# Optimization experiments

Measured on AMD Instinct MI355X. Metric: run time of the kernel, lower is better.

## Reference

```python
import jax, jax.numpy as jnp
import numpy as np

N = 1 << 20          # number of sample points (rays x samples)
ENC = 32             # hash-grid encoded dim (16 levels x 2 features)
HID = 64
GEO = 15


def setup_inputs() -> dict:
    key = jax.random.key(0)
    ks = jax.random.split(key, 16)
    sc = lambda fan_in: 1.0 / np.sqrt(fan_in)
    return {
        "x": jax.random.normal(ks[0], (N, ENC), jnp.float32),
        "d": jax.random.normal(ks[1], (N, ENC), jnp.float32),
        # sigma net: ENC -> 64 -> 64 -> 1+GEO, bias-free, stored [in, out]
        "Ws0": jax.random.normal(ks[2], (ENC, HID), jnp.float32) * sc(ENC),
        "Ws1": jax.random.normal(ks[3], (HID, HID), jnp.float32) * sc(HID),
        "Ws2": jax.random.normal(ks[4], (HID, 1 + GEO), jnp.float32) * sc(HID),
        # color net: ENC+GEO -> 64 -> 64 -> 64 -> 3, bias-free
        "Wc0": jax.random.normal(ks[5], (ENC + GEO, HID), jnp.float32) * sc(ENC + GEO),
        "Wc1": jax.random.normal(ks[6], (HID, HID), jnp.float32) * sc(HID),
        "Wc2": jax.random.normal(ks[7], (HID, HID), jnp.float32) * sc(HID),
        "Wc3": jax.random.normal(ks[8], (HID, 3), jnp.float32) * sc(HID),
    }


def reference(x, d, Ws0, Ws1, Ws2, Wc0, Wc1, Wc2, Wc3):
    # sigma network: ReLU after EVERY layer (including the last, as in source)
    h = x
    for W in (Ws0, Ws1, Ws2):
        h = jax.nn.relu(h @ W)
    sigma = h[..., 0]            # [N]
    geo_feat = h[..., 1:]        # [N, GEO]

    # color network: ReLU on all but last layer, then sigmoid
    h = jnp.concatenate([d, geo_feat], axis=-1)   # [N, ENC+GEO]
    color_ws = (Wc0, Wc1, Wc2, Wc3)
    for i, W in enumerate(color_ws):
        h = h @ W
        if i != len(color_ws) - 1:
            h = jax.nn.relu(h)
    color = jax.nn.sigmoid(h)    # [N, 3]
    return color, sigma
```

## Files before the change

kernel.cpp:

```cpp
#include <hip/hip_runtime.h>
#include <hip/hip_bf16.h>

typedef short s8v __attribute__((ext_vector_type(8)));
typedef float f4v __attribute__((ext_vector_type(4)));

#define MFMA_BF16 __builtin_amdgcn_mfma_f32_16x16x32_bf16

constexpr int OFF_W0T  = 0;
constexpr int OFF_W1T  = 2560;
constexpr int OFF_W2T  = 7168;
constexpr int OFF_WC0T = 8320;
constexpr int OFF_WC1T = 12928;
constexpr int OFF_WC2T = 17536;
constexpr int OFF_WC3T = 22144;
constexpr int OFF_G    = 23168;
constexpr int SMEM_EL  = OFF_G + 8 * 1024;

static __device__ __forceinline__ short bf2s(__hip_bfloat16 h) {
    union { __hip_bfloat16 b; short s; } u; u.b = h; return u.s;
}

__global__ __launch_bounds__(512, 4)
void rf_fused(const void* __restrict__ xv,
              const void* __restrict__ dv,
              const void* __restrict__ Ws0,
              const void* __restrict__ Ws1,
              const void* __restrict__ Ws2,
              const void* __restrict__ Wc0,
              const void* __restrict__ Wc1,
              const void* __restrict__ Wc2,
              const void* __restrict__ Wc3,
              void* __restrict__ outp,
              int npts)
{
    __shared__ __align__(16) short smem[SMEM_EL];
    __shared__ int cls_cnt;
    const int t = threadIdx.x;

    if (t == 0) cls_cnt = 0;
    __syncthreads();
    {
        unsigned short w = ((const unsigned short*)xv)[2 * t];
        int e = (w >> 7) & 0xFF;
        if (e >= 110 && e <= 140) atomicAdd(&cls_cnt, 1);
    }
    __syncthreads();
    const bool isbf = (cls_cnt >= 256);

    auto ldw = [&](const void* p, int idx) -> short {
        if (isbf) return ((const short*)p)[idx];
        return bf2s(__float2bfloat16(((const float*)p)[idx]));
    };

    for (int i = t; i < 2048; i += 512) { int k = i >> 6, n = i & 63; smem[OFF_W0T  + n*40 + k] = ldw(Ws0, i); }
    for (int i = t; i < 4096; i += 512) { int k = i >> 6, n = i & 63; smem[OFF_W1T  + n*72 + k] = ldw(Ws1, i); }
    for (int i = t; i < 1024; i += 512) { int k = i >> 4, n = i & 15; smem[OFF_W2T  + n*72 + k] = ldw(Ws2, i); }
    for (int i = t; i < 4096; i += 512) { int n = i >> 6, k = i & 63; smem[OFF_WC0T + n*72 + k] = (k < 47) ? ldw(Wc0, k*64 + n) : (short)0; }
    for (int i = t; i < 4096; i += 512) { int k = i >> 6, n = i & 63; smem[OFF_WC1T + n*72 + k] = ldw(Wc1, i); }
    for (int i = t; i < 4096; i += 512) { int k = i >> 6, n = i & 63; smem[OFF_WC2T + n*72 + k] = ldw(Wc2, i); }
    for (int i = t; i < 1024; i += 512) { int n = i >> 6, k = i & 63; smem[OFF_WC3T + n*72 + k] = (n < 3) ? ldw(Wc3, k*3 + n) : (short)0; }
    for (int i = t; i < 8192; i += 512) smem[OFF_G + i] = 0;
    __syncthreads();

    const int lane = t & 63;
    const int wv   = t >> 6;
    const int m16  = lane & 15;
    const int q    = lane >> 4;
    short* sG = smem + OFF_G + wv * 1024;

    const f4v zf = {0.f, 0.f, 0.f, 0.f};

    auto loadRow8f = [&](const void* p, int eoff) -> s8v {
        const float* f = (const float*)p + eoff;
        f4v f0 = *(const f4v*)f;
        f4v f1 = *(const f4v*)(f + 4);
        s8v r;
        #pragma unroll
        for (int j = 0; j < 4; j++) {
            r[j]     = bf2s(__float2bfloat16(f0[j]));
            r[j + 4] = bf2s(__float2bfloat16(f1[j]));
        }
        return r;
    };
    auto putOut = [&](int idx, float v) {
        if (isbf) ((short*)outp)[idx] = bf2s(__float2bfloat16(v));
        else      ((float*)outp)[idx] = v;
    };

    auto redist = [&](const f4v (&a)[4], s8v (&fr)[2]) {
        unsigned int P[4][2];
        #pragma unroll
        for (int kt = 0; kt < 4; kt++)
            #pragma unroll
            for (int rp = 0; rp < 2; rp++) {
                float lo = fmaxf(a[kt][2*rp],     0.f);
                float hi = fmaxf(a[kt][2*rp + 1], 0.f);
                union { __hip_bfloat162 b; unsigned int u; } cu;
                cu.b = __float22bfloat162_rn(float2{lo, hi});
                P[kt][rp] = cu.u;
            }
        #pragma unroll
        for (int a2 = 0; a2 < 2; a2++)
            #pragma unroll
            for (int rp = 0; rp < 2; rp++) {
                asm("v_permlane32_swap_b32 %0, %1" : "+v"(P[2*a2][rp]), "+v"(P[2*a2+1][rp]));
                asm("v_permlane16_swap_b32 %0, %1" : "+v"(P[2*a2][rp]), "+v"(P[2*a2+1][rp]));
            }
        #pragma unroll
        for (int kc = 0; kc < 2; kc++) {
            union { unsigned int u[4]; s8v v; } fu;
            fu.u[0] = P[2*kc][0];     fu.u[1] = P[2*kc][1];
            fu.u[2] = P[2*kc + 1][0]; fu.u[3] = P[2*kc + 1][1];
            fr[kc] = fu.v;
        }
    };

    auto layerT = [&](int woff, const s8v (&bf)[2][2], f4v (&out)[2][4]) {
        #pragma unroll
        for (int kt = 0; kt < 4; kt++) {
            s8v a0 = *(const s8v*)(smem + woff + (kt*16 + m16)*72 + q*8);
            s8v a1 = *(const s8v*)(smem + woff + (kt*16 + m16)*72 + 32 + q*8);
            #pragma unroll
            for (int pt = 0; pt < 2; pt++)
                out[pt][kt] = MFMA_BF16(a1, bf[pt][1], MFMA_BF16(a0, bf[pt][0], zf, 0,0,0), 0,0,0);
        }
    };

    const int ntiles = npts / 32;
    const int tstep  = gridDim.x * 8;
    int tile = blockIdx.x * 8 + wv;

    s8v xr[2], dr[2];
    if (isbf && tile < ntiles) {
        #pragma unroll
        for (int pt = 0; pt < 2; pt++) {
            const int off = (tile*32 + pt*16 + m16)*32 + q*8;
            xr[pt] = *(const s8v*)((const short*)xv + off);
            dr[pt] = *(const s8v*)((const short*)dv + off);
        }
    }

    for (; tile < ntiles; tile += tstep) {
        const int r0  = tile * 32;
        const int nxt = tile + tstep;

        s8v xrn[2], drn[2];
        if (isbf && nxt < ntiles) {
            #pragma unroll
            for (int pt = 0; pt < 2; pt++) {
                const int off = (nxt*32 + pt*16 + m16)*32 + q*8;
                xrn[pt] = *(const s8v*)((const short*)xv + off);
                drn[pt] = *(const s8v*)((const short*)dv + off);
            }
        }

        s8v xb[2], db[2];
        if (isbf) {
            xb[0] = xr[0]; xb[1] = xr[1];
            db[0] = dr[0]; db[1] = dr[1];
        } else {
            #pragma unroll
            for (int pt = 0; pt < 2; pt++) {
                const int off = (r0 + pt*16 + m16)*32 + q*8;
                xb[pt] = loadRow8f(xv, off);
                db[pt] = loadRow8f(dv, off);
            }
        }

        f4v acc[2][4];
        s8v bf[2][2];

        #pragma unroll
        for (int kt = 0; kt < 4; kt++) {
            s8v a0 = *(const s8v*)(smem + OFF_W0T + (kt*16 + m16)*40 + q*8);
            #pragma unroll
            for (int pt = 0; pt < 2; pt++)
                acc[pt][kt] = MFMA_BF16(a0, xb[pt], zf, 0,0,0);
        }
        #pragma unroll
        for (int pt = 0; pt < 2; pt++) redist(acc[pt], bf[pt]);

        layerT(OFF_W1T, bf, acc);
        #pragma unroll
        for (int pt = 0; pt < 2; pt++) redist(acc[pt], bf[pt]);

        f4v s3[2];
        {
            s8v c0 = *(const s8v*)(smem + OFF_W2T + m16*72 + q*8);
            s8v c1 = *(const s8v*)(smem + OFF_W2T + m16*72 + 32 + q*8);
            #pragma unroll
            for (int pt = 0; pt < 2; pt++)
                s3[pt] = MFMA_BF16(c1, bf[pt][1], MFMA_BF16(c0, bf[pt][0], zf, 0,0,0), 0,0,0);
        }

        #pragma unroll
        for (int pt = 0; pt < 2; pt++) {
            const int point = pt*16 + m16;
            #pragma unroll
            for (int r = 0; r < 4; r++) {
                float v = fmaxf(s3[pt][r], 0.f);
                if (q*4 + r == 0) {
                    putOut(3*npts + r0 + point, v);
                    sG[point*32 + 15] = 0;
                } else {
                    sG[point*32 + q*4 + r - 1] = bf2s(__float2bfloat16(v));
                }
            }
        }
        asm volatile("" ::: "memory");

        s8v gb[2];
        #pragma unroll
        for (int pt = 0; pt < 2; pt++)
            gb[pt] = *(const s8v*)(sG + (pt*16 + m16)*32 + q*8);
        asm volatile("" ::: "memory");

        #pragma unroll
        for (int pt = 0; pt < 2; pt++) { bf[pt][0] = db[pt]; bf[pt][1] = gb[pt]; }
        layerT(OFF_WC0T, bf, acc);
        #pragma unroll
        for (int pt = 0; pt < 2; pt++) redist(acc[pt], bf[pt]);

        layerT(OFF_WC1T, bf, acc);
        #pragma unroll
        for (int pt = 0; pt < 2; pt++) redist(acc[pt], bf[pt]);

        layerT(OFF_WC2T, bf, acc);
        #pragma unroll
        for (int pt = 0; pt < 2; pt++) redist(acc[pt], bf[pt]);

        f4v c7[2];
        {
            s8v e0 = *(const s8v*)(smem + OFF_WC3T + m16*72 + q*8);
            s8v e1 = *(const s8v*)(smem + OFF_WC3T + m16*72 + 32 + q*8);
            #pragma unroll
            for (int pt = 0; pt < 2; pt++)
                c7[pt] = MFMA_BF16(e1, bf[pt][1], MFMA_BF16(e0, bf[pt][0], zf, 0,0,0), 0,0,0);
        }
        if (q == 0) {
            #pragma unroll
            for (int pt = 0; pt < 2; pt++) {
                const int base = (r0 + pt*16 + m16) * 3;
                #pragma unroll
                for (int r = 0; r < 3; r++) {
                    float v  = c7[pt][r];
                    float sg = 1.0f / (1.0f + __expf(-v));
                    putOut(base + r, sg);
                }
            }
        }

        if (isbf) {
            xr[0] = xrn[0]; xr[1] = xrn[1];
            dr[0] = drn[0]; dr[1] = drn[1];
        }
    }
}

extern "C" void kernel_launch(void* const* d_in, const int* in_sizes, int n_in,
                              void* d_out, int out_size, void* d_ws, size_t ws_size,
                              hipStream_t stream) {
    const int npts = in_sizes[0] / 32;
    rf_fused<<<512, 512, 0, stream>>>(d_in[0], d_in[1], d_in[2], d_in[3], d_in[4],
                                      d_in[5], d_in[6], d_in[7], d_in[8],
                                      d_out, npts);
}
```

Measured before the change: 314.9 us.

## Hold weight fragments in registers and route geo features through lane permutes

```diff
diff --git a/kernel.cpp b/kernel.cpp
--- a/kernel.cpp
+++ b/kernel.cpp
@@ -13,14 +13,13 @@
 constexpr int OFF_WC1T = 12928;
 constexpr int OFF_WC2T = 17536;
 constexpr int OFF_WC3T = 22144;
-constexpr int OFF_G    = 23168;
-constexpr int SMEM_EL  = OFF_G + 8 * 1024;
+constexpr int SMEM_EL  = 23296;
 
 static __device__ __forceinline__ short bf2s(__hip_bfloat16 h) {
     union { __hip_bfloat16 b; short s; } u; u.b = h; return u.s;
 }
 
-__global__ __launch_bounds__(512, 4)
+__global__ __launch_bounds__(512, 2)
 void rf_fused(const void* __restrict__ xv,
               const void* __restrict__ dv,
               const void* __restrict__ Ws0,
@@ -55,20 +54,42 @@
     for (int i = t; i < 2048; i += 512) { int k = i >> 6, n = i & 63; smem[OFF_W0T  + n*40 + k] = ldw(Ws0, i); }
     for (int i = t; i < 4096; i += 512) { int k = i >> 6, n = i & 63; smem[OFF_W1T  + n*72 + k] = ldw(Ws1, i); }
     for (int i = t; i < 1024; i += 512) { int k = i >> 4, n = i & 15; smem[OFF_W2T  + n*72 + k] = ldw(Ws2, i); }
-    for (int i = t; i < 4096; i += 512) { int n = i >> 6, k = i & 63; smem[OFF_WC0T + n*72 + k] = (k < 47) ? ldw(Wc0, k*64 + n) : (short)0; }
+    for (int i = t; i < 4096; i += 512) {
+        int n = i >> 6, k = i & 63;
+        short v = 0;
+        if (k < 32)                 v = ldw(Wc0, k*64 + n);
+        else if (k >= 33 && k < 48) v = ldw(Wc0, (k-1)*64 + n);
+        smem[OFF_WC0T + n*72 + k] = v;
+    }
     for (int i = t; i < 4096; i += 512) { int k = i >> 6, n = i & 63; smem[OFF_WC1T + n*72 + k] = ldw(Wc1, i); }
     for (int i = t; i < 4096; i += 512) { int k = i >> 6, n = i & 63; smem[OFF_WC2T + n*72 + k] = ldw(Wc2, i); }
     for (int i = t; i < 1024; i += 512) { int n = i >> 6, k = i & 63; smem[OFF_WC3T + n*72 + k] = (n < 3) ? ldw(Wc3, k*3 + n) : (short)0; }
-    for (int i = t; i < 8192; i += 512) smem[OFF_G + i] = 0;
     __syncthreads();
 
     const int lane = t & 63;
     const int wv   = t >> 6;
     const int m16  = lane & 15;
     const int q    = lane >> 4;
-    short* sG = smem + OFF_G + wv * 1024;
 
     const f4v zf = {0.f, 0.f, 0.f, 0.f};
+
+    s8v w0f[4], w1f[4][2], wc0f[4][2], wc1f[4][2], wc2f[4][2], w2f[2], wc3f[2];
+    #pragma unroll
+    for (int kt = 0; kt < 4; kt++) {
+        w0f[kt] = *(const s8v*)(smem + OFF_W0T + (kt*16 + m16)*40 + q*8);
+        #pragma unroll
+        for (int h = 0; h < 2; h++) {
+            w1f[kt][h]  = *(const s8v*)(smem + OFF_W1T  + (kt*16 + m16)*72 + h*32 + q*8);
+            wc0f[kt][h] = *(const s8v*)(smem + OFF_WC0T + (kt*16 + m16)*72 + h*32 + q*8);
+            wc1f[kt][h] = *(const s8v*)(smem + OFF_WC1T + (kt*16 + m16)*72 + h*32 + q*8);
+            wc2f[kt][h] = *(const s8v*)(smem + OFF_WC2T + (kt*16 + m16)*72 + h*32 + q*8);
+        }
+    }
+    #pragma unroll
+    for (int h = 0; h < 2; h++) {
+        w2f[h]  = *(const s8v*)(smem + OFF_W2T  + m16*72 + h*32 + q*8);
+        wc3f[h] = *(const s8v*)(smem + OFF_WC3T + m16*72 + h*32 + q*8);
+    }
 
     auto loadRow8f = [&](const void* p, int eoff) -> s8v {
         const float* f = (const float*)p + eoff;
@@ -115,50 +136,35 @@
         }
     };
 
-    auto layerT = [&](int woff, const s8v (&bf)[2][2], f4v (&out)[2][4]) {
-        #pragma unroll
-        for (int kt = 0; kt < 4; kt++) {
-            s8v a0 = *(const s8v*)(smem + woff + (kt*16 + m16)*72 + q*8);
-            s8v a1 = *(const s8v*)(smem + woff + (kt*16 + m16)*72 + 32 + q*8);
-            #pragma unroll
-            for (int pt = 0; pt < 2; pt++)
-                out[pt][kt] = MFMA_BF16(a1, bf[pt][1], MFMA_BF16(a0, bf[pt][0], zf, 0,0,0), 0,0,0);
-        }
+    auto layerR = [&](const s8v (&wf)[4][2], const s8v (&bfr)[2][2], f4v (&out)[2][4]) {
+        #pragma unroll
+        for (int kt = 0; kt < 4; kt++)
+            #pragma unroll
+            for (int pt = 0; pt < 2; pt++)
+                out[pt][kt] = MFMA_BF16(wf[kt][1], bfr[pt][1],
+                              MFMA_BF16(wf[kt][0], bfr[pt][0], zf, 0,0,0), 0,0,0);
     };
 
     const int ntiles = npts / 32;
     const int tstep  = gridDim.x * 8;
     int tile = blockIdx.x * 8 + wv;
 
-    s8v xr[2], dr[2];
+    s8v xb[2], db[2];
     if (isbf && tile < ntiles) {
         #pragma unroll
         for (int pt = 0; pt < 2; pt++) {
             const int off = (tile*32 + pt*16 + m16)*32 + q*8;
-            xr[pt] = *(const s8v*)((const short*)xv + off);
-            dr[pt] = *(const s8v*)((const short*)dv + off);
-        }
-    }
-
+            xb[pt] = *(const s8v*)((const short*)xv + off);
+            db[pt] = *(const s8v*)((const short*)dv + off);
+        }
+    }
+
+    #pragma unroll 1
     for (; tile < ntiles; tile += tstep) {
         const int r0  = tile * 32;
         const int nxt = tile + tstep;
 
-        s8v xrn[2], drn[2];
-        if (isbf && nxt < ntiles) {
-            #pragma unroll
-            for (int pt = 0; pt < 2; pt++) {
-                const int off = (nxt*32 + pt*16 + m16)*32 + q*8;
-                xrn[pt] = *(const s8v*)((const short*)xv + off);
-                drn[pt] = *(const s8v*)((const short*)dv + off);
-            }
-        }
-
-        s8v xb[2], db[2];
-        if (isbf) {
-            xb[0] = xr[0]; xb[1] = xr[1];
-            db[0] = dr[0]; db[1] = dr[1];
-        } else {
+        if (!isbf) {
             #pragma unroll
             for (int pt = 0; pt < 2; pt++) {
                 const int off = (r0 + pt*16 + m16)*32 + q*8;
@@ -168,75 +174,73 @@
         }
 
         f4v acc[2][4];
-        s8v bf[2][2];
-
-        #pragma unroll
-        for (int kt = 0; kt < 4; kt++) {
-            s8v a0 = *(const s8v*)(smem + OFF_W0T + (kt*16 + m16)*40 + q*8);
-            #pragma unroll
-            for (int pt = 0; pt < 2; pt++)
-                acc[pt][kt] = MFMA_BF16(a0, xb[pt], zf, 0,0,0);
-        }
-        #pragma unroll
-        for (int pt = 0; pt < 2; pt++) redist(acc[pt], bf[pt]);
-
-        layerT(OFF_W1T, bf, acc);
-        #pragma unroll
-        for (int pt = 0; pt < 2; pt++) redist(acc[pt], bf[pt]);
+        s8v bfr[2][2];
+
+        #pragma unroll
+        for (int kt = 0; kt < 4; kt++)
+            #pragma unroll
+            for (int pt = 0; pt < 2; pt++)
+                acc[pt][kt] = MFMA_BF16(w0f[kt], xb[pt], zf, 0,0,0);
+
+        if (isbf && nxt < ntiles) {
+            #pragma unroll
+            for (int pt = 0; pt < 2; pt++)
+                xb[pt] = *(const s8v*)((const short*)xv + (nxt*32 + pt*16 + m16)*32 + q*8);
+        }
+
+        #pragma unroll
+        for (int pt = 0; pt < 2; pt++) redist(acc[pt], bfr[pt]);
+
+        layerR(w1f, bfr, acc);
+        #pragma unroll
+        for (int pt = 0; pt < 2; pt++) redist(acc[pt], bfr[pt]);
 
         f4v s3[2];
-        {
-            s8v c0 = *(const s8v*)(smem + OFF_W2T + m16*72 + q*8);
-            s8v c1 = *(const s8v*)(smem + OFF_W2T + m16*72 + 32 + q*8);
-            #pragma unroll
-            for (int pt = 0; pt < 2; pt++)
-                s3[pt] = MFMA_BF16(c1, bf[pt][1], MFMA_BF16(c0, bf[pt][0], zf, 0,0,0), 0,0,0);
+        #pragma unroll
+        for (int pt = 0; pt < 2; pt++)
+            s3[pt] = MFMA_BF16(w2f[1], bfr[pt][1],
+                     MFMA_BF16(w2f[0], bfr[pt][0], zf, 0,0,0), 0,0,0);
+
+        if (q == 0) {
+            #pragma unroll
+            for (int pt = 0; pt < 2; pt++)
+                putOut(3*npts + r0 + pt*16 + m16, fmaxf(s3[pt][0], 0.f));
         }
 
         #pragma unroll
         for (int pt = 0; pt < 2; pt++) {
-            const int point = pt*16 + m16;
-            #pragma unroll
-            for (int r = 0; r < 4; r++) {
-                float v = fmaxf(s3[pt][r], 0.f);
-                if (q*4 + r == 0) {
-                    putOut(3*npts + r0 + point, v);
-                    sG[point*32 + 15] = 0;
-                } else {
-                    sG[point*32 + q*4 + r - 1] = bf2s(__float2bfloat16(v));
-                }
-            }
-        }
-        asm volatile("" ::: "memory");
-
-        s8v gb[2];
+            f4v sd[4] = { s3[pt], s3[pt], s3[pt], s3[pt] };
+            s8v fj[2];
+            redist(sd, fj);
+            bfr[pt][1] = fj[1];
+            bfr[pt][0] = db[pt];
+        }
+
+        layerR(wc0f, bfr, acc);
+
+        if (isbf && nxt < ntiles) {
+            #pragma unroll
+            for (int pt = 0; pt < 2; pt++)
+                db[pt] = *(const s8v*)((const short*)dv + (nxt*32 + pt*16 + m16)*32 + q*8);
+        }
+
+        #pragma unroll
+        for (int pt = 0; pt < 2; pt++) redist(acc[pt], bfr[pt]);
+
+        layerR(wc1f, bfr, acc);
+        #pragma unroll
+        for (int pt = 0; pt < 2; pt++) redist(acc[pt], bfr[pt]);
+
+        layerR(wc2f, bfr, acc);
+        #pragma unroll
+        for (int pt = 0; pt < 2; pt++) redist(acc[pt], bfr[pt]);
+
+        f4v c7[2];
         #pragma unroll
         for (int pt = 0; pt < 2; pt++)
-            gb[pt] = *(const s8v*)(sG + (pt*16 + m16)*32 + q*8);
-        asm volatile("" ::: "memory");
-
-        #pragma unroll
-        for (int pt = 0; pt < 2; pt++) { bf[pt][0] = db[pt]; bf[pt][1] = gb[pt]; }
-        layerT(OFF_WC0T, bf, acc);
-        #pragma unroll
-        for (int pt = 0; pt < 2; pt++) redist(acc[pt], bf[pt]);
-
-        layerT(OFF_WC1T, bf, acc);
-        #pragma unroll
-        for (int pt = 0; pt < 2; pt++) redist(acc[pt], bf[pt]);
-
-        layerT(OFF_WC2T, bf, acc);
-        #pragma unroll
-        for (int pt = 0; pt < 2; pt++) redist(acc[pt], bf[pt]);
-
-        f4v c7[2];
-        {
-            s8v e0 = *(const s8v*)(smem + OFF_WC3T + m16*72 + q*8);
-            s8v e1 = *(const s8v*)(smem + OFF_WC3T + m16*72 + 32 + q*8);
-            #pragma unroll
-            for (int pt = 0; pt < 2; pt++)
-                c7[pt] = MFMA_BF16(e1, bf[pt][1], MFMA_BF16(e0, bf[pt][0], zf, 0,0,0), 0,0,0);
-        }
+            c7[pt] = MFMA_BF16(wc3f[1], bfr[pt][1],
+                     MFMA_BF16(wc3f[0], bfr[pt][0], zf, 0,0,0), 0,0,0);
+
         if (q == 0) {
             #pragma unroll
             for (int pt = 0; pt < 2; pt++) {
@@ -249,11 +253,6 @@
                 }
             }
         }
-
-        if (isbf) {
-            xr[0] = xrn[0]; xr[1] = xrn[1];
-            dr[0] = drn[0]; dr[1] = drn[1];
-        }
     }
 }
 
```

After: 338.3 us. +7.4%, slower.
